# Performance work log

Measured on AMD Instinct MI355X. Metric: run time of the kernel, lower is better.

The kernel has to match this reference:

```python
import jax, jax.numpy as jnp
import numpy as np
from jax import lax

B, H, W = 32, 80, 80
K = 100                        # max_candidates
THRESH = 0.1                   # minutiae_threshold
DIST_T = 16.0
ANGLE_T = np.pi / 6.0
PI = np.pi


def _gauss_kernel1d(ks, sigma):
    c = jnp.arange(ks, dtype=jnp.float32) - ks // 2
    g = jnp.exp(-(c * c) / (2.0 * sigma * sigma))
    return g / g.sum()


def _gaussian_blur(img):  # [B,1,H,W], separable 5x5 sigma=1.5
    k = _gauss_kernel1d(5, 1.5)
    dn = ('NCHW', 'OIHW', 'NCHW')
    x = lax.conv_general_dilated(img, k.reshape(1, 1, 1, 5), (1, 1), [(0, 0), (2, 2)], dimension_numbers=dn)
    x = lax.conv_general_dilated(x, k.reshape(1, 1, 5, 1), (1, 1), [(2, 2), (0, 0)], dimension_numbers=dn)
    return x


def _up8(m):  # nearest-neighbor x8 upsample on last two dims
    return jnp.repeat(jnp.repeat(m, 8, axis=-2), 8, axis=-1)


def _detect_and_nms(score, ori, xoff, yoff):
    # score [H,W]; ori [90,H,W]; xoff/yoff [8,H,W]
    vals, idx = lax.top_k(score.reshape(-1), K)   # sorted descending == argsort by score
    valid = vals > THRESH
    rows = idx // W
    cols = idx % W
    ang_idx = jnp.argmax(ori[:, rows, cols], axis=0)   # [K]
    xo = jnp.argmax(xoff[:, rows, cols], axis=0)
    yo = jnp.argmax(yoff[:, rows, cols], axis=0)
    angles = (ang_idx.astype(jnp.float32) * 2.0 - 89.0) * (PI / 180.0)
    x = cols.astype(jnp.float32) * 8.0 + xo.astype(jnp.float32)
    y = rows.astype(jnp.float32) * 8.0 + yo.astype(jnp.float32)
    mnt = jnp.stack([x, y, angles, vals], axis=-1)     # [K,4]
    # pairwise suppression mask (cdist + circular angle delta)
    d2 = jnp.sum((mnt[:, None, :2] - mnt[None, :, :2]) ** 2, axis=-1)
    dist = jnp.sqrt(d2)
    ad = jnp.abs(angles[:, None] - angles[None, :])
    am = jnp.minimum(ad, 2.0 * PI - ad)
    sup = (dist < DIST_T) & (am < ANGLE_T)
    ar = jnp.arange(K)
    def body(i, keep):
        s = sup[i] & (ar > i)
        return jnp.where(keep[i], keep & ~s, keep)
    keep = lax.fori_loop(0, K, body, valid)
    return mnt, keep


def setup_inputs() -> dict:
    key = jax.random.key(0)
    ks = jax.random.split(key, 7)
    return {
        'segmentation': jax.random.uniform(ks[0], (B, 1, H, W), jnp.float32),
        'minutiae_score': jax.random.uniform(ks[1], (B, 1, H, W), jnp.float32),
        'minutiae_orientation': jax.random.normal(ks[2], (B, 90, H, W), jnp.float32),
        'minutiae_x_offset': jax.random.normal(ks[3], (B, 8, H, W), jnp.float32),
        'minutiae_y_offset': jax.random.normal(ks[4], (B, 8, H, W), jnp.float32),
        'orientation': jax.random.normal(ks[5], (B, 90, H, W), jnp.float32),
        'enhanced_real': jax.random.normal(ks[6], (B, 1, 8 * H, 8 * W), jnp.float32),
    }


def reference(segmentation, minutiae_score, minutiae_orientation,
              minutiae_x_offset, minutiae_y_offset, orientation, enhanced_real):
    # --- segmentation mask: round -> gaussian blur -> round
    cleaned = jnp.round(_gaussian_blur(jnp.round(segmentation[:, 0])[:, None]))[:, 0]  # [B,H,W]
    cleaned_up = _up8(cleaned)                                                          # [B,8H,8W]
    # --- minutiae detection (threshold via masked top-k) + sequential NMS
    score = minutiae_score[:, 0] * cleaned
    mnt, keep = jax.vmap(_detect_and_nms)(score, minutiae_orientation,
                                          minutiae_x_offset, minutiae_y_offset)
    # --- orientation field
    ori_idx = jnp.argmax(orientation, axis=1).astype(jnp.float32)   # [B,H,W]
    ori_field = (_up8(ori_idx) * 2.0 - 89.0) * (PI / 180.0) * cleaned_up
    # --- enhanced image: mask + per-image min-max normalize to [0,255]
    enh = enhanced_real[:, 0] * cleaned_up
    ef = enh.reshape(B, -1)
    emin = jnp.min(ef, axis=1, keepdims=True)
    emax = jnp.max(ef, axis=1, keepdims=True)
    enorm = (ef - emin) / (emax - emin + 1e-8)
    enh_visual = enorm.reshape(B, 8 * H, 8 * W) * 255.0
    return (mnt, keep.astype(jnp.float32), enh_visual, cleaned_up * 255.0, ori_field)
```

## Files before the change

kernel.cpp:

```cpp
#include <hip/hip_runtime.h>
#include <math.h>

#define BN  32
#define H   80
#define W   80
#define HW  6400
#define KC  100
#define NCH 90
#define UW  640
#define UHW 409600

static constexpr size_t OUT_MNT   = 0;
static constexpr size_t OUT_KEEP  = (size_t)BN * KC * 4;
static constexpr size_t OUT_ENH   = OUT_KEEP + (size_t)BN * KC;
static constexpr size_t OUT_CLEAN = OUT_ENH + (size_t)BN * UHW;
static constexpr size_t OUT_ORI   = OUT_CLEAN + (size_t)BN * UHW;

#define PI_F 3.14159265358979323846
#define MM_BLOCKS 64
#define ORI_MEGA  400
#define CAP 2048

typedef float vfloat4 __attribute__((ext_vector_type(4)));

__device__ __forceinline__ unsigned enc_f(float f) {
    unsigned u = __float_as_uint(f);
    return (u & 0x80000000u) ? ~u : (u | 0x80000000u);
}
__device__ __forceinline__ float dec_f(unsigned k) {
    return (k & 0x80000000u) ? __uint_as_float(k ^ 0x80000000u) : __uint_as_float(~k);
}
__device__ __forceinline__ unsigned long long shflx(unsigned long long v, int off) {
    unsigned hi = (unsigned)__shfl_xor((int)(unsigned)(v >> 32), off);
    unsigned lo = (unsigned)__shfl_xor((int)(unsigned)(v & 0xffffffffull), off);
    return ((unsigned long long)hi << 32) | lo;
}

__global__ __launch_bounds__(512) void k_clean(const float* __restrict__ seg,
                                               float* __restrict__ cleaned_g) {
    __shared__ float s_in[HW];
    __shared__ float s_h[HW];
    const int b = blockIdx.x, tid = threadIdx.x;

    float g[5];
    {
        float s = 0.f;
        #pragma unroll
        for (int i = 0; i < 5; i++) {
            float c = (float)(i - 2);
            g[i] = expf(-(c * c) / 4.5f);
            s += g[i];
        }
        #pragma unroll
        for (int i = 0; i < 5; i++) g[i] /= s;
    }

    for (int i = tid; i < HW; i += 512) s_in[i] = rintf(seg[(size_t)b * HW + i]);
    __syncthreads();
    for (int i = tid; i < HW; i += 512) {
        int h = i / W, w = i % W;
        float acc = 0.f;
        #pragma unroll
        for (int dx = -2; dx <= 2; dx++) {
            int ww = w + dx;
            if (ww >= 0 && ww < W) acc += s_in[h * W + ww] * g[dx + 2];
        }
        s_h[i] = acc;
    }
    __syncthreads();
    for (int i = tid; i < HW; i += 512) {
        int h = i / W, w = i % W;
        float acc = 0.f;
        #pragma unroll
        for (int dy = -2; dy <= 2; dy++) {
            int hh = h + dy;
            if (hh >= 0 && hh < H) acc += s_h[hh * W + w] * g[dy + 2];
        }
        cleaned_g[(size_t)b * HW + i] = rintf(acc);
    }
}

__global__ __launch_bounds__(512) void k_mega(const float* __restrict__ mscore,
                                              const float* __restrict__ cleaned,
                                              const float* __restrict__ ori,
                                              const float* __restrict__ enh,
                                              float* __restrict__ ori_idx,
                                              float* __restrict__ pmin,
                                              float* __restrict__ pmax,
                                              int* __restrict__ ws_idx,
                                              float* __restrict__ ws_val) {
    __shared__ __align__(16) char um[20480];
    __shared__ unsigned long long s_sel[KC];
    __shared__ unsigned s_rm[HW / 32];
    __shared__ int s_cnt[5];
    __shared__ int s_n;
    __shared__ float s_T;
    __shared__ int s_mode;
    __shared__ float smin[8], smax[8];

    const int bx = blockIdx.x, tid = threadIdx.x;
    const int lane = tid & 63;

    if (bx < BN) {
        unsigned long long* s_cand = (unsigned long long*)um;
        unsigned long long* s_red  = (unsigned long long*)um + CAP;
        const int b = bx;

        if (tid < HW / 32) s_rm[tid] = 0u;
        if (tid < 5) s_cnt[tid] = 0;
        __syncthreads();

        float sc[13];
        #pragma unroll
        for (int j = 0; j < 13; j++) {
            int i = j * 512 + tid;
            sc[j] = (i < HW) ? mscore[(size_t)b * HW + i] * cleaned[(size_t)b * HW + i]
                             : -1.0f;
        }

        int c0 = 0, c1 = 0, c2 = 0, c3 = 0, c4 = 0;
        #pragma unroll
        for (int j = 0; j < 13; j++) {
            float v = sc[j];
            c0 += (v > 0.95f); c1 += (v > 0.9f); c2 += (v > 0.8f);
            c3 += (v > 0.5f);  c4 += (v > 0.0f);
        }
        #pragma unroll
        for (int off = 32; off > 0; off >>= 1) {
            c0 += __shfl_xor(c0, off); c1 += __shfl_xor(c1, off);
            c2 += __shfl_xor(c2, off); c3 += __shfl_xor(c3, off);
            c4 += __shfl_xor(c4, off);
        }
        if (lane == 0) {
            atomicAdd(&s_cnt[0], c0); atomicAdd(&s_cnt[1], c1);
            atomicAdd(&s_cnt[2], c2); atomicAdd(&s_cnt[3], c3);
            atomicAdd(&s_cnt[4], c4);
        }
        __syncthreads();

        if (tid == 0) {
            int n95 = s_cnt[0], n90 = s_cnt[1], n80 = s_cnt[2], n50 = s_cnt[3], n0 = s_cnt[4];
            int mode; float T = 0.f;
            if (n0 < KC)                      { mode = 1; }
            else if (n95 >= KC && n95 <= CAP) { mode = 0; T = 0.95f; }
            else if (n90 >= KC && n90 <= CAP) { mode = 0; T = 0.9f; }
            else if (n80 >= KC && n80 <= CAP) { mode = 0; T = 0.8f; }
            else if (n50 >= KC && n50 <= CAP) { mode = 0; T = 0.5f; }
            else if (n0 <= CAP)               { mode = 0; T = 0.0f; }
            else                              { mode = 2; }
            s_mode = mode; s_T = T; s_n = 0;
        }
        __syncthreads();
        const int mode = s_mode;

        if (mode != 2) {
            const float T = s_T;
            #pragma unroll
            for (int j = 0; j < 13; j++) {
                int i = j * 512 + tid;
                bool take = (mode == 0) ? (sc[j] > T)
                                        : (sc[j] > 0.f || (i < 256 && sc[j] == 0.0f));
                if (take) {
                    int pos = atomicAdd(&s_n, 1);
                    s_cand[pos] = ((unsigned long long)enc_f(sc[j]) << 32) | (unsigned)(HW - i);
                }
            }
            __syncthreads();
            const int n = s_n;
            for (int c = tid; c < n; c += 512) {
                unsigned long long kk = s_cand[c];
                int rank = 0;
                for (int m = 0; m < n; m++) rank += (s_cand[m] > kk) ? 1 : 0;
                if (rank < KC) s_sel[rank] = kk;
            }
            __syncthreads();
        } else {
            for (int k = 0; k < KC; k++) {
                unsigned long long lmax = 0ull;
                #pragma unroll
                for (int j = 0; j < 13; j++) {
                    int i = j * 512 + tid;
                    if (i < HW && sc[j] >= 0.f && !((s_rm[i >> 5] >> (i & 31)) & 1u)) {
                        unsigned long long kk =
                            ((unsigned long long)enc_f(sc[j]) << 32) | (unsigned)(HW - i);
                        if (kk > lmax) lmax = kk;
                    }
                }
                s_red[tid] = lmax;
                __syncthreads();
                for (int off = 256; off > 0; off >>= 1) {
                    if (tid < off) {
                        unsigned long long o = s_red[tid + off];
                        if (o > s_red[tid]) s_red[tid] = o;
                    }
                    __syncthreads();
                }
                if (tid == 0) {
                    unsigned long long wkey = s_red[0];
                    s_sel[k] = wkey;
                    int wi = HW - (int)(wkey & 0xffffffffull);
                    s_rm[wi >> 5] |= 1u << (wi & 31);
                }
                __syncthreads();
            }
        }

        if (tid < KC) {
            unsigned long long e = s_sel[tid];
            ws_idx[(size_t)b * KC + tid] = HW - (int)(e & 0xffffffffull);
            ws_val[(size_t)b * KC + tid] = dec_f((unsigned)(e >> 32));
        }
    } else if (bx < BN + ORI_MEGA) {
        float4* s_bv = (float4*)um;
        float4* s_bj = (float4*)um + 512;
        const int grp = tid >> 7, ln = tid & 127;
        const int p4 = (bx - BN) * 128 + ln;
        const int b = p4 / (HW / 4), pp = p4 % (HW / 4);
        const float4* o = (const float4*)(ori + (size_t)b * NCH * HW) + pp;
        const int cs = (grp * NCH) >> 2, ce = ((grp + 1) * NCH) >> 2;

        float4 bv = o[(size_t)cs * (HW / 4)];
        float4 bj = make_float4((float)cs, (float)cs, (float)cs, (float)cs);
        for (int j = cs + 1; j < ce; j++) {
            float4 v = o[(size_t)j * (HW / 4)];
            if (v.x > bv.x) { bv.x = v.x; bj.x = (float)j; }
            if (v.y > bv.y) { bv.y = v.y; bj.y = (float)j; }
            if (v.z > bv.z) { bv.z = v.z; bj.z = (float)j; }
            if (v.w > bv.w) { bv.w = v.w; bj.w = (float)j; }
        }
        s_bv[tid] = bv; s_bj[tid] = bj;
        __syncthreads();
        if (grp == 0) {
            #pragma unroll
            for (int g = 1; g < 4; g++) {
                float4 v = s_bv[g * 128 + ln], jx = s_bj[g * 128 + ln];
                if (v.x > bv.x) { bv.x = v.x; bj.x = jx.x; }
                if (v.y > bv.y) { bv.y = v.y; bj.y = jx.y; }
                if (v.z > bv.z) { bv.z = v.z; bj.z = jx.z; }
                if (v.w > bv.w) { bv.w = v.w; bj.w = jx.w; }
            }
            ((float4*)ori_idx)[p4] = bj;
        }
    } else {
        const int mb = bx - (BN + ORI_MEGA);
        const int b = mb >> 6, chunk = mb & 63;
        const float4* e4 = (const float4*)(enh + (size_t)b * UHW);
        const float* cb = cleaned + (size_t)b * HW;

        float vmin = INFINITY, vmax = -INFINITY;
        for (int i = chunk * 512 + tid; i < UHW / 4; i += MM_BLOCKS * 512) {
            float4 v = e4[i];
            int p = i * 4;
            int Y = p / UW, X = p % UW;
            float c = cb[(Y >> 3) * W + (X >> 3)];
            float a = v.x * c, bb = v.y * c, cc = v.z * c, dd = v.w * c;
            vmin = fminf(vmin, fminf(fminf(a, bb), fminf(cc, dd)));
            vmax = fmaxf(vmax, fmaxf(fmaxf(a, bb), fmaxf(cc, dd)));
        }
        #pragma unroll
        for (int off = 32; off > 0; off >>= 1) {
            vmin = fminf(vmin, __shfl_xor(vmin, off));
            vmax = fmaxf(vmax, __shfl_xor(vmax, off));
        }
        int wave = tid >> 6;
        if (lane == 0) { smin[wave] = vmin; smax[wave] = vmax; }
        __syncthreads();
        if (tid == 0) {
            float m0 = smin[0], m1 = smax[0];
            #pragma unroll
            for (int wv = 1; wv < 8; wv++) {
                m0 = fminf(m0, smin[wv]);
                m1 = fmaxf(m1, smax[wv]);
            }
            pmin[b * MM_BLOCKS + chunk] = m0;
            pmax[b * MM_BLOCKS + chunk] = m1;
        }
    }
}

__global__ __launch_bounds__(256) void k_final(const float* __restrict__ enh,
                                               const float* __restrict__ cleaned,
                                               const float* __restrict__ ori_idx,
                                               const float* __restrict__ pmin,
                                               const float* __restrict__ pmax,
                                               float* __restrict__ out) {
    __shared__ float s_emin, s_emax;
    const int b = blockIdx.x / 400;
    if (threadIdx.x < 64) {
        float vmin = pmin[b * MM_BLOCKS + threadIdx.x];
        float vmax = pmax[b * MM_BLOCKS + threadIdx.x];
        #pragma unroll
        for (int off = 32; off > 0; off >>= 1) {
            vmin = fminf(vmin, __shfl_xor(vmin, off));
            vmax = fmaxf(vmax, __shfl_xor(vmax, off));
        }
        if (threadIdx.x == 0) { s_emin = vmin; s_emax = vmax; }
    }
    __syncthreads();

    int t4 = blockIdx.x * 256 + threadIdx.x;
    int p4 = t4 % (UHW / 4);
    int p = p4 * 4;
    int Y = p / UW, X = p % UW;
    int cidx = b * HW + (Y >> 3) * W + (X >> 3);
    float c  = cleaned[cidx];
    float oi = ori_idx[cidx];
    float emin = s_emin, emax = s_emax;
    float inv = 255.0f / (emax - emin + 1e-8f);

    float4 e = ((const float4*)enh)[t4];
    vfloat4 ev;
    ev.x = (e.x * c - emin) * inv;
    ev.y = (e.y * c - emin) * inv;
    ev.z = (e.z * c - emin) * inv;
    ev.w = (e.w * c - emin) * inv;

    float cv = c * 255.0f;
    float ov = (oi * 2.0f - 89.0f) * (float)(PI_F / 180.0) * c;
    vfloat4 cvv = {cv, cv, cv, cv};
    vfloat4 ovv = {ov, ov, ov, ov};

    __builtin_nontemporal_store(ev,  ((vfloat4*)(out + OUT_ENH))   + t4);
    __builtin_nontemporal_store(cvv, ((vfloat4*)(out + OUT_CLEAN)) + t4);
    __builtin_nontemporal_store(ovv, ((vfloat4*)(out + OUT_ORI))   + t4);
}

__global__ __launch_bounds__(256) void k_gather(const float* __restrict__ mori,
                                                const float* __restrict__ mxo,
                                                const float* __restrict__ myo,
                                                const int* __restrict__ ws_idx,
                                                const float* __restrict__ ws_val,
                                                float* __restrict__ out) {
    int wid = blockIdx.x * 4 + (threadIdx.x >> 6);
    int lane = threadIdx.x & 63;
    int b = wid / KC, k = wid % KC;
    int idx = ws_idx[(size_t)b * KC + k];

    const float* pm = mori + (size_t)b * NCH * HW + idx;
    unsigned long long kk =
        ((unsigned long long)enc_f(pm[(size_t)lane * HW]) << 32) | (unsigned)(127 - lane);
    if (lane < NCH - 64) {
        unsigned long long k1 =
            ((unsigned long long)enc_f(pm[(size_t)(64 + lane) * HW]) << 32) | (unsigned)(127 - (64 + lane));
        if (k1 > kk) kk = k1;
    }
    unsigned long long kx = 0ull, ky = 0ull;
    if (lane >= 32 && lane < 40)
        kx = ((unsigned long long)enc_f(mxo[((size_t)b * 8 + (lane - 32)) * HW + idx]) << 32)
             | (unsigned)(15 - (lane - 32));
    if (lane >= 40 && lane < 48)
        ky = ((unsigned long long)enc_f(myo[((size_t)b * 8 + (lane - 40)) * HW + idx]) << 32)
             | (unsigned)(15 - (lane - 40));

    #pragma unroll
    for (int off = 32; off > 0; off >>= 1) {
        unsigned long long o;
        o = shflx(kk, off); if (o > kk) kk = o;
        o = shflx(kx, off); if (o > kx) kx = o;
        o = shflx(ky, off); if (o > ky) ky = o;
    }

    if (lane == 0) {
        int ch = 127 - (int)(kk & 0xffffffffull);
        int xo = 15  - (int)(kx & 0xffffffffull);
        int yo = 15  - (int)(ky & 0xffffffffull);
        int r = idx / W, c = idx % W;
        float4 m;
        m.x = (float)c * 8.0f + (float)xo;
        m.y = (float)r * 8.0f + (float)yo;
        m.z = ((float)ch * 2.0f - 89.0f) * (float)(PI_F / 180.0);
        m.w = ws_val[(size_t)b * KC + k];
        ((float4*)(out + OUT_MNT))[(size_t)b * KC + k] = m;
    }
}

__global__ __launch_bounds__(64) void k_nms(float* __restrict__ out) {
    const int b = blockIdx.x, l = threadIdx.x;
    const float4* mnt = (const float4*)(out + OUT_MNT) + (size_t)b * KC;
    float4 m0 = mnt[l];
    bool has1 = (l + 64) < KC;
    float4 m1 = has1 ? mnt[l + 64] : make_float4(0.f, 0.f, 0.f, -1.f);
    int keep0 = (m0.w > 0.1f) ? 1 : 0;
    int keep1 = (has1 && m1.w > 0.1f) ? 1 : 0;

    for (int i = 0; i < KC; i++) {
        bool hi = i >= 64;
        int src = i & 63;
        float xi = __shfl(hi ? m1.x : m0.x, src);
        float yi = __shfl(hi ? m1.y : m0.y, src);
        float ai = __shfl(hi ? m1.z : m0.z, src);
        int   ki = __shfl(hi ? keep1 : keep0, src);
        if (ki) {
            if (keep0 && l > i) {
                float dx = xi - m0.x, dy = yi - m0.y;
                float dist = sqrtf(dx * dx + dy * dy);
                float ad = fabsf(ai - m0.z);
                float am = fminf(ad, (float)(2.0 * PI_F) - ad);
                if (dist < 16.0f && am < (float)(PI_F / 6.0)) keep0 = 0;
            }
            if (keep1 && (l + 64) > i) {
                float dx = xi - m1.x, dy = yi - m1.y;
                float dist = sqrtf(dx * dx + dy * dy);
                float ad = fabsf(ai - m1.z);
                float am = fminf(ad, (float)(2.0 * PI_F) - ad);
                if (dist < 16.0f && am < (float)(PI_F / 6.0)) keep1 = 0;
            }
        }
    }
    out[OUT_KEEP + (size_t)b * KC + l] = (float)keep0;
    if (has1) out[OUT_KEEP + (size_t)b * KC + 64 + l] = (float)keep1;
}

extern "C" void kernel_launch(void* const* d_in, const int* in_sizes, int n_in,
                              void* d_out, int out_size, void* d_ws, size_t ws_size,
                              hipStream_t stream) {
    const float* seg    = (const float*)d_in[0];
    const float* mscore = (const float*)d_in[1];
    const float* mori   = (const float*)d_in[2];
    const float* mxo    = (const float*)d_in[3];
    const float* myo    = (const float*)d_in[4];
    const float* ori    = (const float*)d_in[5];
    const float* enh    = (const float*)d_in[6];
    float* out = (float*)d_out;

    float* cleaned = (float*)d_ws;
    float* ori_idx = cleaned + (size_t)BN * HW;
    float* pmin    = ori_idx + (size_t)BN * HW;
    float* pmax    = pmin + (size_t)BN * MM_BLOCKS;
    int*   ws_idx  = (int*)(pmax + (size_t)BN * MM_BLOCKS);
    float* ws_val  = (float*)(ws_idx + (size_t)BN * KC);

    const int nBig4 = (BN * UHW / 4) / 256;
    const int nMega = BN + ORI_MEGA + BN * MM_BLOCKS;

    k_clean<<<BN, 512, 0, stream>>>(seg, cleaned);
    k_mega<<<nMega, 512, 0, stream>>>(mscore, cleaned, ori, enh,
                                      ori_idx, pmin, pmax, ws_idx, ws_val);
    k_final<<<nBig4, 256, 0, stream>>>(enh, cleaned, ori_idx, pmin, pmax, out);
    k_gather<<<(BN * KC) / 4, 256, 0, stream>>>(mori, mxo, myo, ws_idx, ws_val, out);
    k_nms<<<BN, 64, 0, stream>>>(out);
}
```

Measured before the change: 105.5 us.

## Split blur into row bands and fuse gather with final write kernel

The segmentation blur kernel now runs one block per 8-row band with a 2-row halo, giving 320 blocks instead of 32. The gather and final normalize/write kernels are merged into one launch, with the first 800 blocks doing the gather and the rest doing the full-resolution writes. This removes one kernel launch and lets the gather run alongside the bandwidth-heavy writes. The cost is some halo rows loaded and blurred redundantly per band, plus a branch on block index.

```diff
diff --git a/kernel.cpp b/kernel.cpp
--- a/kernel.cpp
+++ b/kernel.cpp
@@ -20,6 +20,8 @@
 #define MM_BLOCKS 64
 #define ORI_MEGA  400
 #define CAP 2048
+#define GAT_BLOCKS 800
+#define FIN_BLOCKS 12800
 
 typedef float vfloat4 __attribute__((ext_vector_type(4)));
 
@@ -38,9 +40,12 @@
 
 __global__ __launch_bounds__(512) void k_clean(const float* __restrict__ seg,
                                                float* __restrict__ cleaned_g) {
-    __shared__ float s_in[HW];
-    __shared__ float s_h[HW];
-    const int b = blockIdx.x, tid = threadIdx.x;
+    __shared__ float s_in[12 * 80];
+    __shared__ float s_h[12 * 80];
+    const int blk = blockIdx.x;
+    const int b = blk / 10, band = blk % 10;
+    const int r0 = band * 8 - 2;
+    const int tid = threadIdx.x;
 
     float g[5];
     {
@@ -55,28 +60,29 @@
         for (int i = 0; i < 5; i++) g[i] /= s;
     }
 
-    for (int i = tid; i < HW; i += 512) s_in[i] = rintf(seg[(size_t)b * HW + i]);
+    for (int i = tid; i < 12 * 80; i += 512) {
+        int lr = i / 80, w = i % 80;
+        int gr = r0 + lr;
+        s_in[i] = (gr >= 0 && gr < H) ? rintf(seg[(size_t)b * HW + gr * W + w]) : 0.f;
+    }
     __syncthreads();
-    for (int i = tid; i < HW; i += 512) {
-        int h = i / W, w = i % W;
+    for (int i = tid; i < 12 * 80; i += 512) {
+        int lr = i / 80, w = i % 80;
         float acc = 0.f;
         #pragma unroll
         for (int dx = -2; dx <= 2; dx++) {
             int ww = w + dx;
-            if (ww >= 0 && ww < W) acc += s_in[h * W + ww] * g[dx + 2];
+            if (ww >= 0 && ww < W) acc += s_in[lr * 80 + ww] * g[dx + 2];
         }
         s_h[i] = acc;
     }
     __syncthreads();
-    for (int i = tid; i < HW; i += 512) {
-        int h = i / W, w = i % W;
+    for (int i = tid; i < 8 * 80; i += 512) {
+        int k = i / 80, w = i % 80;
         float acc = 0.f;
         #pragma unroll
-        for (int dy = -2; dy <= 2; dy++) {
-            int hh = h + dy;
-            if (hh >= 0 && hh < H) acc += s_h[hh * W + w] * g[dy + 2];
-        }
-        cleaned_g[(size_t)b * HW + i] = rintf(acc);
+        for (int dy = 0; dy < 5; dy++) acc += s_h[(k + dy) * 80 + w] * g[dy];
+        cleaned_g[(size_t)b * HW + (band * 8 + k) * W + w] = rintf(acc);
     }
 }
 
@@ -278,99 +284,103 @@
     }
 }
 
-__global__ __launch_bounds__(256) void k_final(const float* __restrict__ enh,
-                                               const float* __restrict__ cleaned,
-                                               const float* __restrict__ ori_idx,
-                                               const float* __restrict__ pmin,
-                                               const float* __restrict__ pmax,
-                                               float* __restrict__ out) {
-    __shared__ float s_emin, s_emax;
-    const int b = blockIdx.x / 400;
-    if (threadIdx.x < 64) {
-        float vmin = pmin[b * MM_BLOCKS + threadIdx.x];
-        float vmax = pmax[b * MM_BLOCKS + threadIdx.x];
+__global__ __launch_bounds__(256) void k_fg(const float* __restrict__ enh,
+                                            const float* __restrict__ cleaned,
+                                            const float* __restrict__ ori_idx,
+                                            const float* __restrict__ pmin,
+                                            const float* __restrict__ pmax,
+                                            const float* __restrict__ mori,
+                                            const float* __restrict__ mxo,
+                                            const float* __restrict__ myo,
+                                            const int* __restrict__ ws_idx,
+                                            const float* __restrict__ ws_val,
+                                            float* __restrict__ out) {
+    const int bx = blockIdx.x, tid = threadIdx.x;
+
+    if (bx < GAT_BLOCKS) {
+        const int lane = tid & 63;
+        const int wid = bx * 4 + (tid >> 6);
+        const int b = wid / KC, k = wid % KC;
+        const int idx = ws_idx[(size_t)b * KC + k];
+
+        const float* pm = mori + (size_t)b * NCH * HW + idx;
+        unsigned long long kk =
+            ((unsigned long long)enc_f(pm[(size_t)lane * HW]) << 32) | (unsigned)(127 - lane);
+        if (lane < NCH - 64) {
+            unsigned long long k1 =
+                ((unsigned long long)enc_f(pm[(size_t)(64 + lane) * HW]) << 32)
+                | (unsigned)(127 - (64 + lane));
+            if (k1 > kk) kk = k1;
+        }
+        unsigned long long kx = 0ull, ky = 0ull;
+        if (lane >= 32 && lane < 40)
+            kx = ((unsigned long long)enc_f(mxo[((size_t)b * 8 + (lane - 32)) * HW + idx]) << 32)
+                 | (unsigned)(15 - (lane - 32));
+        if (lane >= 40 && lane < 48)
+            ky = ((unsigned long long)enc_f(myo[((size_t)b * 8 + (lane - 40)) * HW + idx]) << 32)
+                 | (unsigned)(15 - (lane - 40));
+
         #pragma unroll
         for (int off = 32; off > 0; off >>= 1) {
-            vmin = fminf(vmin, __shfl_xor(vmin, off));
-            vmax = fmaxf(vmax, __shfl_xor(vmax, off));
-        }
-        if (threadIdx.x == 0) { s_emin = vmin; s_emax = vmax; }
-    }
-    __syncthreads();
-
-    int t4 = blockIdx.x * 256 + threadIdx.x;
-    int p4 = t4 % (UHW / 4);
-    int p = p4 * 4;
-    int Y = p / UW, X = p % UW;
-    int cidx = b * HW + (Y >> 3) * W + (X >> 3);
-    float c  = cleaned[cidx];
-    float oi = ori_idx[cidx];
-    float emin = s_emin, emax = s_emax;
-    float inv = 255.0f / (emax - emin + 1e-8f);
-
-    float4 e = ((const float4*)enh)[t4];
-    vfloat4 ev;
-    ev.x = (e.x * c - emin) * inv;
-    ev.y = (e.y * c - emin) * inv;
-    ev.z = (e.z * c - emin) * inv;
-    ev.w = (e.w * c - emin) * inv;
-
-    float cv = c * 255.0f;
-    float ov = (oi * 2.0f - 89.0f) * (float)(PI_F / 180.0) * c;
-    vfloat4 cvv = {cv, cv, cv, cv};
-    vfloat4 ovv = {ov, ov, ov, ov};
-
-    __builtin_nontemporal_store(ev,  ((vfloat4*)(out + OUT_ENH))   + t4);
-    __builtin_nontemporal_store(cvv, ((vfloat4*)(out + OUT_CLEAN)) + t4);
-    __builtin_nontemporal_store(ovv, ((vfloat4*)(out + OUT_ORI))   + t4);
-}
-
-__global__ __launch_bounds__(256) void k_gather(const float* __restrict__ mori,
-                                                const float* __restrict__ mxo,
-                                                const float* __restrict__ myo,
-                                                const int* __restrict__ ws_idx,
-                                                const float* __restrict__ ws_val,
-                                                float* __restrict__ out) {
-    int wid = blockIdx.x * 4 + (threadIdx.x >> 6);
-    int lane = threadIdx.x & 63;
-    int b = wid / KC, k = wid % KC;
-    int idx = ws_idx[(size_t)b * KC + k];
-
-    const float* pm = mori + (size_t)b * NCH * HW + idx;
-    unsigned long long kk =
-        ((unsigned long long)enc_f(pm[(size_t)lane * HW]) << 32) | (unsigned)(127 - lane);
-    if (lane < NCH - 64) {
-        unsigned long long k1 =
-            ((unsigned long long)enc_f(pm[(size_t)(64 + lane) * HW]) << 32) | (unsigned)(127 - (64 + lane));
-        if (k1 > kk) kk = k1;
-    }
-    unsigned long long kx = 0ull, ky = 0ull;
-    if (lane >= 32 && lane < 40)
-        kx = ((unsigned long long)enc_f(mxo[((size_t)b * 8 + (lane - 32)) * HW + idx]) << 32)
-             | (unsigned)(15 - (lane - 32));
-    if (lane >= 40 && lane < 48)
-        ky = ((unsigned long long)enc_f(myo[((size_t)b * 8 + (lane - 40)) * HW + idx]) << 32)
-             | (unsigned)(15 - (lane - 40));
-
-    #pragma unroll
-    for (int off = 32; off > 0; off >>= 1) {
-        unsigned long long o;
-        o = shflx(kk, off); if (o > kk) kk = o;
-        o = shflx(kx, off); if (o > kx) kx = o;
-        o = shflx(ky, off); if (o > ky) ky = o;
-    }
-
-    if (lane == 0) {
-        int ch = 127 - (int)(kk & 0xffffffffull);
-        int xo = 15  - (int)(kx & 0xffffffffull);
-        int yo = 15  - (int)(ky & 0xffffffffull);
-        int r = idx / W, c = idx % W;
-        float4 m;
-        m.x = (float)c * 8.0f + (float)xo;
-        m.y = (float)r * 8.0f + (float)yo;
-        m.z = ((float)ch * 2.0f - 89.0f) * (float)(PI_F / 180.0);
-        m.w = ws_val[(size_t)b * KC + k];
-        ((float4*)(out + OUT_MNT))[(size_t)b * KC + k] = m;
+            unsigned long long o;
+            o = shflx(kk, off); if (o > kk) kk = o;
+            o = shflx(kx, off); if (o > kx) kx = o;
+            o = shflx(ky, off); if (o > ky) ky = o;
+        }
+
+        if (lane == 0) {
+            int ch = 127 - (int)(kk & 0xffffffffull);
+            int xo = 15  - (int)(kx & 0xffffffffull);
+            int yo = 15  - (int)(ky & 0xffffffffull);
+            int r = idx / W, c = idx % W;
+            float4 m;
+            m.x = (float)c * 8.0f + (float)xo;
+            m.y = (float)r * 8.0f + (float)yo;
+            m.z = ((float)ch * 2.0f - 89.0f) * (float)(PI_F / 180.0);
+            m.w = ws_val[(size_t)b * KC + k];
+            ((float4*)(out + OUT_MNT))[(size_t)b * KC + k] = m;
+        }
+    } else {
+        __shared__ float s_emin, s_emax;
+        const int fb = bx - GAT_BLOCKS;
+        const int b = fb / 400;
+        if (tid < 64) {
+            float vmin = pmin[b * MM_BLOCKS + tid];
+            float vmax = pmax[b * MM_BLOCKS + tid];
+            #pragma unroll
+            for (int off = 32; off > 0; off >>= 1) {
+                vmin = fminf(vmin, __shfl_xor(vmin, off));
+                vmax = fmaxf(vmax, __shfl_xor(vmax, off));
+            }
+            if (tid == 0) { s_emin = vmin; s_emax = vmax; }
+        }
+        __syncthreads();
+
+        int t4 = fb * 256 + tid;
+        int p4 = t4 % (UHW / 4);
+        int p = p4 * 4;
+        int Y = p / UW, X = p % UW;
+        int cidx = b * HW + (Y >> 3) * W + (X >> 3);
+        float c  = cleaned[cidx];
+        float oi = ori_idx[cidx];
+        float emin = s_emin, emax = s_emax;
+        float inv = 255.0f / (emax - emin + 1e-8f);
+
+        float4 e = ((const float4*)enh)[t4];
+        vfloat4 ev;
+        ev.x = (e.x * c - emin) * inv;
+        ev.y = (e.y * c - emin) * inv;
+        ev.z = (e.z * c - emin) * inv;
+        ev.w = (e.w * c - emin) * inv;
+
+        float cv = c * 255.0f;
+        float ov = (oi * 2.0f - 89.0f) * (float)(PI_F / 180.0) * c;
+        vfloat4 cvv = {cv, cv, cv, cv};
+        vfloat4 ovv = {ov, ov, ov, ov};
+
+        __builtin_nontemporal_store(ev,  ((vfloat4*)(out + OUT_ENH))   + t4);
+        __builtin_nontemporal_store(cvv, ((vfloat4*)(out + OUT_CLEAN)) + t4);
+        __builtin_nontemporal_store(ovv, ((vfloat4*)(out + OUT_ORI))   + t4);
     }
 }
 
@@ -430,13 +440,13 @@
     int*   ws_idx  = (int*)(pmax + (size_t)BN * MM_BLOCKS);
     float* ws_val  = (float*)(ws_idx + (size_t)BN * KC);
 
-    const int nBig4 = (BN * UHW / 4) / 256;
     const int nMega = BN + ORI_MEGA + BN * MM_BLOCKS;
-
-    k_clean<<<BN, 512, 0, stream>>>(seg, cleaned);
+    const int nFG   = GAT_BLOCKS + FIN_BLOCKS;
+
+    k_clean<<<BN * 10, 512, 0, stream>>>(seg, cleaned);
     k_mega<<<nMega, 512, 0, stream>>>(mscore, cleaned, ori, enh,
                                       ori_idx, pmin, pmax, ws_idx, ws_val);
-    k_final<<<nBig4, 256, 0, stream>>>(enh, cleaned, ori_idx, pmin, pmax, out);
-    k_gather<<<(BN * KC) / 4, 256, 0, stream>>>(mori, mxo, myo, ws_idx, ws_val, out);
+    k_fg<<<nFG, 256, 0, stream>>>(enh, cleaned, ori_idx, pmin, pmax,
+                                  mori, mxo, myo, ws_idx, ws_val, out);
     k_nms<<<BN, 64, 0, stream>>>(out);
 }
```

After: 95.15 us. -9.8%, faster.
